# Kernel tuning notes

Measured on AMD Instinct MI355X. Metric: run time of the kernel, lower is better.

## Reference

```python
import jax, jax.numpy as jnp
import numpy as np

# ---- db4 filters (pywt conventions: dec_lo = rec_lo[::-1], rec_hi = qmf(rec_lo)) ----
F = 8  # db4 filter length
_rec_lo = np.array([0.23037781330885523, 0.7148465705525415, 0.6308807679295904,
                    -0.027983769416983849, -0.18703481171888114, 0.030841381835986965,
                    0.032883011666982945, -0.010597401784997278], dtype=np.float32)
_rec_hi = _rec_lo[::-1].copy()
_rec_hi[1::2] *= -1.0
REC_LO = jnp.asarray(_rec_lo)
REC_HI = jnp.asarray(_rec_hi)

MAX_LEVEL = 9  # pywt.dwt_max_level(4096, 8)


def _conv1d(x, kernel, stride=1, padding='VALID', lhs_dilation=None):
    # x: [B, L] -> correlation (XLA conv does NOT flip the kernel)
    out = jax.lax.conv_general_dilated(
        x[:, None, :], kernel[None, None, :],
        window_strides=(stride,), padding=padding,
        lhs_dilation=lhs_dilation,
        dimension_numbers=('NCH', 'OIH', 'NCH'))
    return out[:, 0, :]


def dwt(x):
    # pywt.dwt(x, 'db4', mode='symmetric'):
    # cA = np.convolve(sym_ext(x, F-1), dec_lo, 'valid')[1::2]
    # convolution with dec filter == correlation with rec filter (its reverse)
    ext = jnp.pad(x, ((0, 0), (F - 1, F - 1)), mode='symmetric')[:, 1:]
    return _conv1d(ext, REC_LO, stride=2), _conv1d(ext, REC_HI, stride=2)


def idwt(ca, cd):
    # pywt.idwt: zero-upsample coeffs, full convolution with rec filters, trim edges
    n = ca.shape[1]
    pad = ((F - 1, F - 1),)
    out = (_conv1d(ca, REC_LO[::-1], padding=pad, lhs_dilation=(2,)) +
           _conv1d(cd, REC_HI[::-1], padding=pad, lhs_dilation=(2,)))
    return out[:, F - 2:2 * n]  # output length = 2n - F + 2


def wavelet_features(x1):
    # Faithful to WaveletDWTLayer stack + WaveletParsingLayer: at each level k>=2,
    # reconstruct with details of levels k and k-1 only (others zeroed), with
    # pywt.waverec's trim-by-one rule; concatenate the 8 full-length reconstructions.
    a = x1
    cds, recs = [], []
    for level in range(1, MAX_LEVEL + 1):
        a, d = dwt(a)
        if level >= 2:
            r = idwt(jnp.zeros_like(d), d)
            for j in range(level - 2, -1, -1):
                dj = cds[j] if j == level - 2 else jnp.zeros_like(cds[j])
                if r.shape[1] == dj.shape[1] + 1:  # waverec trim rule
                    r = r[:, :-1]
                r = idwt(r, dj)
            recs.append(r)  # [B, signal_length]
        cds.append(d)
    return jnp.concatenate(recs, axis=1)  # [B, signal_length*(MAX_LEVEL-1)]


def reference(x1, x2, x3, W0, b0, W1, b1, W2, b2):
    # x2/x3 are placeholders in the original module (overwritten by layers 1/2)
    h = wavelet_features(x1)
    for W, b in ((W0, b0), (W1, b1), (W2, b2)):
        h = jax.nn.relu(h) @ W.T + b
    return h


def setup_inputs() -> dict:
    key = jax.random.key(0)
    ks = jax.random.split(key, 4)
    B, N = 2048, 4096
    D_IN, H1, H2, OUT = 32768, 181, 13, 10
    return {
        'x1': jax.random.normal(ks[0], (B, N), jnp.float32),
        'x2': jnp.zeros((B, 1, 8), jnp.float32),
        'x3': jnp.zeros((B, 1, 8), jnp.float32),
        'W0': jax.random.normal(ks[1], (H1, D_IN), jnp.float32) / np.float32(np.sqrt(D_IN)),
        'b0': jnp.zeros((H1,), jnp.float32),
        'W1': jax.random.normal(ks[2], (H2, H1), jnp.float32) / np.float32(np.sqrt(H1)),
        'b1': jnp.zeros((H2,), jnp.float32),
        'W2': jax.random.normal(ks[3], (OUT, H2), jnp.float32) / np.float32(np.sqrt(H2)),
        'b2': jnp.zeros((OUT,), jnp.float32),
    }
```

## Files before the change

### kernel.cpp

```cpp
#include <hip/hip_runtime.h>
#include <hip/hip_bf16.h>


typedef _Float16 f16x8 __attribute__((ext_vector_type(8)));
typedef _Float16 f16x4v __attribute__((ext_vector_type(4)));
typedef float f32x4 __attribute__((ext_vector_type(4)));

#define WV_THREADS 256
#define DROW 4144

#define L0 0.23037781330885523f
#define L1 0.7148465705525415f
#define L2f 0.6308807679295904f
#define L3 -0.02798376941698385f
#define L4 -0.18703481171888114f
#define L5 0.030841381835986965f
#define L6 0.032883011666982945f
#define L7 -0.010597401784997278f

#define H0 -0.010597401784997278f
#define H1 -0.032883011666982945f
#define H2 0.030841381835986965f
#define H3 0.18703481171888114f
#define H4 -0.02798376941698385f
#define H5 -0.6308807679295904f
#define H6 0.7148465705525415f
#define H7 -0.23037781330885523f

__device__ __forceinline__ int ext_idx(int j, int n) {
  return (j < 6) ? (5 - j) : ((j < n + 6) ? (j - 6) : (2 * n + 5 - j));
}

__device__ __forceinline__ void dwt2(const float* a, float* anext, float* d,
                                     int n, int m, bool store_a) {
  const int ng = (m + 1) >> 1;
  for (int g = threadIdx.x; g < ng; g += WV_THREADS) {
    float w[10];
    if (g >= 2 && 4 * g + 9 <= n + 5) {
      const float2* af = (const float2*)a + (2 * g - 3);
      float2 b0 = af[0], b1 = af[1], b2 = af[2], b3 = af[3], b4 = af[4];
      w[0] = b0.x; w[1] = b0.y; w[2] = b1.x; w[3] = b1.y; w[4] = b2.x;
      w[5] = b2.y; w[6] = b3.x; w[7] = b3.y; w[8] = b4.x; w[9] = b4.y;
    } else {
#pragma unroll
      for (int q = 0; q < 10; ++q) {
        int j = 4 * g + q;
        int jm = n + 12;
        if (j > jm) j = jm;
        w[q] = a[ext_idx(j, n)];
      }
    }
    float sl0 = w[0]*L0 + w[1]*L1 + w[2]*L2f + w[3]*L3 + w[4]*L4 + w[5]*L5 + w[6]*L6 + w[7]*L7;
    float sh0 = w[0]*H0 + w[1]*H1 + w[2]*H2  + w[3]*H3 + w[4]*H4 + w[5]*H5 + w[6]*H6 + w[7]*H7;
    float sl1 = w[2]*L0 + w[3]*L1 + w[4]*L2f + w[5]*L3 + w[6]*L4 + w[7]*L5 + w[8]*L6 + w[9]*L7;
    float sh1 = w[2]*H0 + w[3]*H1 + w[4]*H2  + w[5]*H3 + w[6]*H4 + w[7]*H5 + w[8]*H6 + w[9]*H7;
    if (2 * g + 1 < m) {
      if (store_a) *(float2*)(anext + 2 * g) = make_float2(sl0, sl1);
      *(float2*)(d + 2 * g) = make_float2(sh0, sh1);
    } else {
      if (store_a) anext[2 * g] = sl0;
      d[2 * g] = sh0;
    }
  }
}

template <bool HAS_CA, bool HAS_CD, bool FINAL>
__device__ __forceinline__ void idwt2(const float* ca, const float* cd,
                                      float* outl, _Float16* outg, int dlen) {
  const int npair = dlen - 3;
  const int ng = (npair + 1) >> 1;
  for (int g = threadIdx.x; g < ng; g += WV_THREADS) {
    float e0 = 0.f, o0 = 0.f, e1 = 0.f, o1 = 0.f;
    if (HAS_CA) {
      const float2* f = (const float2*)ca + g;
      float2 a0 = f[0], a1 = f[1], a2 = f[2];
      e0 = a1.y*L0 + a1.x*L2f + a0.y*L4 + a0.x*L6;
      o0 = a1.y*L1 + a1.x*L3  + a0.y*L5 + a0.x*L7;
      e1 = a2.x*L0 + a1.y*L2f + a1.x*L4 + a0.y*L6;
      o1 = a2.x*L1 + a1.y*L3  + a1.x*L5 + a0.y*L7;
    }
    if (HAS_CD) {
      const float2* f = (const float2*)cd + g;
      float2 d0 = f[0], d1 = f[1], d2 = f[2];
      e0 += d1.y*H0 + d1.x*H2 + d0.y*H4 + d0.x*H6;
      o0 += d1.y*H1 + d1.x*H3 + d0.y*H5 + d0.x*H7;
      e1 += d2.x*H0 + d1.y*H2 + d1.x*H4 + d0.y*H6;
      o1 += d2.x*H1 + d1.y*H3 + d1.x*H5 + d0.y*H7;
    }
    bool full = (2 * g + 1 < npair);
    if (FINAL) {
      if (full) {
        f16x4v h;
        h[0] = (_Float16)fmaxf(e0, 0.f); h[1] = (_Float16)fmaxf(o0, 0.f);
        h[2] = (_Float16)fmaxf(e1, 0.f); h[3] = (_Float16)fmaxf(o1, 0.f);
        *(f16x4v*)(outg + 4 * g) = h;
      } else {
        outg[4 * g]     = (_Float16)fmaxf(e0, 0.f);
        outg[4 * g + 1] = (_Float16)fmaxf(o0, 0.f);
      }
    } else {
      if (full) *(float4*)(outl + 4 * g) = make_float4(e0, o0, e1, o1);
      else      *(float2*)(outl + 4 * g) = make_float2(e0, o0);
    }
  }
}

__global__ __launch_bounds__(WV_THREADS) void wv_analysis_cvt(
    const float* __restrict__ x, float* __restrict__ dG,
    const float* __restrict__ W0, _Float16* __restrict__ Bw) {
  __shared__ float r1[4104];
  __shared__ float r2[2056];
  const int tid = threadIdx.x;

  if (blockIdx.x >= 2048) {
    size_t i = ((size_t)(blockIdx.x - 2048) * 256 + tid) * 4;
    int rowc = (int)(i >> 15);
    f16x4v h;
    if (rowc < 181) {
      const float4 v = *(const float4*)(W0 + i);
      h[0] = (_Float16)v.x; h[1] = (_Float16)v.y;
      h[2] = (_Float16)v.z; h[3] = (_Float16)v.w;
    } else {
      h[0] = (_Float16)0.f; h[1] = (_Float16)0.f;
      h[2] = (_Float16)0.f; h[3] = (_Float16)0.f;
    }
    *(f16x4v*)(Bw + i) = h;
    return;
  }

  const int NLa[10]  = {4096, 2051, 1029, 518, 262, 134, 70, 38, 22, 14};
  const int DOFF[10] = {0, 0, 2052, 3082, 3600, 3862, 3996, 4066, 4104, 4126};
  const int LOFF[10] = {0, 0, 1036, 520, 2068, 1040, 2332, 1176, 2404, 1216};
  const int row = blockIdx.x;

  const float4* xr = (const float4*)(x + (size_t)row * 4096);
  for (int i = tid; i < 1024; i += WV_THREADS) ((float4*)r1)[i] = xr[i];
  __syncthreads();

  float* dr = dG + (size_t)row * DROW;
  dwt2(r1, r2, dr + DOFF[1], NLa[0], NLa[1], true);
  __syncthreads();
  const float* ap = r2;
  float* an = r1;
  for (int lev = 2; lev <= 9; ++lev) {
    float* dbuf = ((lev & 1) ? r2 : r1) + LOFF[lev];
    dwt2(ap, an, dbuf, NLa[lev - 1], NLa[lev], lev < 9);
    __syncthreads();
    const float* t = ap; ap = an; an = (float*)t;
  }
  for (int lev = 2; lev <= 9; ++lev) {
    const float* src = ((lev & 1) ? r2 : r1) + LOFF[lev];
    float* dst = dr + DOFF[lev];
    for (int i = tid; i < NLa[lev]; i += WV_THREADS) dst[i] = src[i];
  }
}

__global__ __launch_bounds__(WV_THREADS, 6) void wv_synth(
    const float* __restrict__ dG, _Float16* __restrict__ A) {
  __shared__ float s1[2052];
  __shared__ float s2[2052];
  const int NLa[10]  = {4096, 2051, 1029, 518, 262, 134, 70, 38, 22, 14};
  const int DOFF[10] = {0, 0, 2052, 3082, 3600, 3862, 3996, 4066, 4104, 4126};
  const int row = blockIdx.x;
  const int L = 2 + blockIdx.y;
  const int tid = threadIdx.x;
  const float* dr = dG + (size_t)row * DROW;

  float* cur = s1;
  float* nxt = s2;
  int startj = L - 2;
  if (L >= 6) {
    if (tid < 64) {
      idwt2<false, true, false>(nullptr, dr + DOFF[L], cur, nullptr, NLa[L]);
      asm volatile("s_waitcnt lgkmcnt(0)" ::: "memory");
      for (int j = L - 2; j >= 5; --j) {
        if (j == L - 2)
          idwt2<true, true, false>(cur, dr + DOFF[j + 1], nxt, nullptr, NLa[j + 1]);
        else
          idwt2<true, false, false>(cur, nullptr, nxt, nullptr, NLa[j + 1]);
        asm volatile("s_waitcnt lgkmcnt(0)" ::: "memory");
        float* t = cur; cur = nxt; nxt = t;
      }
    } else {
      for (int j = L - 2; j >= 5; --j) { float* t = cur; cur = nxt; nxt = t; }
    }
    __syncthreads();
    startj = 4;
  } else {
    idwt2<false, true, false>(nullptr, dr + DOFF[L], cur, nullptr, NLa[L]);
    __syncthreads();
  }
  for (int j = startj; j >= 1; --j) {
    if (j == L - 2)
      idwt2<true, true, false>(cur, dr + DOFF[j + 1], nxt, nullptr, NLa[j + 1]);
    else
      idwt2<true, false, false>(cur, nullptr, nxt, nullptr, NLa[j + 1]);
    __syncthreads();
    float* t = cur; cur = nxt; nxt = t;
  }
  _Float16* og = A + (size_t)row * 32768 + (size_t)(L - 2) * 4096;
  if (L == 2)
    idwt2<true, true, true>(cur, dr + DOFF[1], nullptr, og, 2051);
  else
    idwt2<true, false, true>(cur, nullptr, nullptr, og, 2051);
}

__device__ __forceinline__ void load_lds16(const void* g, void* l) {
  __builtin_amdgcn_global_load_lds((__attribute__((address_space(1))) unsigned int*)g,
                                   (__attribute__((address_space(3))) unsigned int*)l,
                                   16, 0, 0);
}

__global__ __launch_bounds__(256, 2) void gemm_kernel(
    const _Float16* __restrict__ A, const _Float16* __restrict__ Bw,
    float* __restrict__ P, int kchunk) {
  __shared__ _Float16 As[128 * 64];
  __shared__ _Float16 Bs[192 * 64];
  const int tid = threadIdx.x;
  const int lane = tid & 63;
  const int wave = tid >> 6;
  const int m0 = blockIdx.x * 128;
  const int k0 = blockIdx.y * kchunk;
  const int nstages = kchunk >> 6;

  f32x4 acc[2][12];
#pragma unroll
  for (int mt = 0; mt < 2; ++mt)
#pragma unroll
    for (int nt = 0; nt < 12; ++nt) acc[mt][nt] = (f32x4){0.f, 0.f, 0.f, 0.f};

  for (int ks = 0; ks < nstages; ++ks) {
    const int kbase = k0 + (ks << 6);
    __syncthreads();
#pragma unroll
    for (int t = 0; t < 4; ++t) {
      int g = ((wave * 4 + t) << 6) + lane;
      int r = g >> 3, cs = g & 7;
      const _Float16* gp = A + (size_t)(m0 + r) * 32768 + kbase + ((cs ^ (r & 7)) << 3);
      load_lds16(gp, (char*)As + (size_t)((wave * 4 + t) << 10));
    }
#pragma unroll
    for (int t = 0; t < 6; ++t) {
      int g = ((wave * 6 + t) << 6) + lane;
      int r = g >> 3, cs = g & 7;
      const _Float16* gp = Bw + (size_t)r * 32768 + kbase + ((cs ^ (r & 7)) << 3);
      load_lds16(gp, (char*)Bs + (size_t)((wave * 6 + t) << 10));
    }
    __syncthreads();
#pragma unroll
    for (int kk = 0; kk < 2; ++kk) {
      const int chunk = kk * 4 + (lane >> 4);
      f16x8 af[2];
#pragma unroll
      for (int mt = 0; mt < 2; ++mt) {
        int r = wave * 32 + mt * 16 + (lane & 15);
        af[mt] = *(const f16x8*)(As + r * 64 + ((chunk ^ (r & 7)) << 3));
      }
#pragma unroll
      for (int nt = 0; nt < 12; ++nt) {
        int rb = nt * 16 + (lane & 15);
        f16x8 bf = *(const f16x8*)(Bs + rb * 64 + ((chunk ^ (rb & 7)) << 3));
        acc[0][nt] = __builtin_amdgcn_mfma_f32_16x16x32_f16(af[0], bf, acc[0][nt], 0, 0, 0);
        acc[1][nt] = __builtin_amdgcn_mfma_f32_16x16x32_f16(af[1], bf, acc[1][nt], 0, 0, 0);
      }
    }
  }
  float* Pp = P + ((size_t)blockIdx.y * 2048 + m0) * 192;
#pragma unroll
  for (int mt = 0; mt < 2; ++mt)
#pragma unroll
    for (int nt = 0; nt < 12; ++nt)
#pragma unroll
      for (int r4 = 0; r4 < 4; ++r4) {
        int rr = wave * 32 + mt * 16 + ((lane >> 4) << 2) + r4;
        int cc = nt * 16 + (lane & 15);
        Pp[(size_t)rr * 192 + cc] = acc[mt][nt][r4];
      }
}

__global__ __launch_bounds__(256) void mlp_kernel(
    const float* __restrict__ P, const float* __restrict__ b0,
    const float* __restrict__ W1, const float* __restrict__ b1,
    const float* __restrict__ W2, const float* __restrict__ b2,
    float* __restrict__ out, int nsplit) {
  __shared__ float part[4][193];
  __shared__ float h1[192];
  __shared__ float h2[13];
  const int row = blockIdx.x;
  const int t = threadIdx.x;
  const int g = t >> 6;
  const int l = t & 63;

  float a0 = 0.f, a1 = 0.f, a2 = 0.f;
  const int per = nsplit >> 2;
  for (int si = 0; si < per; ++si) {
    int s = g + (si << 2);
    const float* Pr = P + ((size_t)s * 2048 + row) * 192;
    a0 += Pr[l]; a1 += Pr[64 + l]; a2 += Pr[128 + l];
  }
  part[g][l] = a0; part[g][64 + l] = a1; part[g][128 + l] = a2;
  __syncthreads();

  if (t < 192) {
    float v = part[0][t] + part[1][t] + part[2][t] + part[3][t];
    h1[t] = (t < 181) ? fmaxf(v + b0[t], 0.f) : 0.f;
  }
  __syncthreads();

#pragma unroll
  for (int r = 0; r < 4; ++r) {
    int j = g + (r << 2);
    if (j < 13) {
      float v = 0.f;
#pragma unroll
      for (int q = 0; q < 3; ++q) {
        int n = l + (q << 6);
        if (n < 181) v += h1[n] * W1[j * 181 + n];
      }
      for (int off = 32; off >= 1; off >>= 1) v += __shfl_down(v, off);
      if (l == 0) h2[j] = fmaxf(v + b1[j], 0.f);
    }
  }
  __syncthreads();

  if (t < 10) {
    float c = b2[t];
#pragma unroll
    for (int j = 0; j < 13; ++j) c += h2[j] * W2[t * 13 + j];
    out[(size_t)row * 10 + t] = c;
  }
}

extern "C" void kernel_launch(void* const* d_in, const int* in_sizes, int n_in,
                              void* d_out, int out_size, void* d_ws, size_t ws_size,
                              hipStream_t stream) {
  const float* x1 = (const float*)d_in[0];
  const float* W0 = (const float*)d_in[3];
  const float* b0 = (const float*)d_in[4];
  const float* W1 = (const float*)d_in[5];
  const float* b1 = (const float*)d_in[6];
  const float* W2 = (const float*)d_in[7];
  const float* b2 = (const float*)d_in[8];
  float* out = (float*)d_out;

  char* ws = (char*)d_ws;
  const size_t A_BYTES = (size_t)2048 * 32768 * 2;
  const size_t B_BYTES = (size_t)192 * 32768 * 2;
  _Float16* Afeat = (_Float16*)ws;
  _Float16* Bw = (_Float16*)(ws + A_BYTES);
  float* Dq = (float*)(ws + A_BYTES + B_BYTES);
  float* P = (float*)(ws + A_BYTES + B_BYTES);

  int nsplit = 32;
  while (nsplit > 1 &&
         A_BYTES + B_BYTES + (size_t)nsplit * 2048 * 192 * 4 > ws_size)
    nsplit >>= 1;

  wv_analysis_cvt<<<2048 + 6144, WV_THREADS, 0, stream>>>(x1, Dq, W0, Bw);
  dim3 sg(2048, 8);
  wv_synth<<<sg, WV_THREADS, 0, stream>>>(Dq, Afeat);
  dim3 gg(16, nsplit);
  gemm_kernel<<<gg, 256, 0, stream>>>(Afeat, Bw, P, 32768 / nsplit);
  mlp_kernel<<<2048, 256, 0, stream>>>(P, b0, W1, b1, W2, b2, out, nsplit);
}
```

Baseline: 228.2 us.

## Fix GEMM split-K at 16 with swizzled block mapping, simplify synth, vectorize copies

Several changes land together. The GEMM split-K factor is now a compile-time constant of 16, replacing the runtime choice that picked up to 32 splits, and launches a 1D grid whose block index is remapped so consecutive blocks share an M tile across K chunks. The mlp kernel reads that constant too. The wavelet synthesis drops its single-wave path for deep levels and runs all levels with the full block, and the detail-coefficient copy in analysis now uses float2 stores. Fewer splits shrink the partial-sum traffic and the reduction work but give the GEMM fewer blocks (256) to spread across the GPU.

After: 243.1 us. 6.5% more time.

```diff
diff --git a/kernel.cpp b/kernel.cpp
--- a/kernel.cpp
+++ b/kernel.cpp
@@ -8,6 +8,8 @@
 
 #define WV_THREADS 256
 #define DROW 4144
+#define NSPLIT 16
+#define KCHUNK 2048
 
 #define L0 0.23037781330885523f
 #define L1 0.7148465705525415f
@@ -151,7 +153,10 @@
   for (int lev = 2; lev <= 9; ++lev) {
     const float* src = ((lev & 1) ? r2 : r1) + LOFF[lev];
     float* dst = dr + DOFF[lev];
-    for (int i = tid; i < NLa[lev]; i += WV_THREADS) dst[i] = src[i];
+    const int n = NLa[lev];
+    for (int i = 2 * tid; i + 1 < n; i += 2 * WV_THREADS)
+      *(float2*)(dst + i) = *(const float2*)(src + i);
+    if ((n & 1) && tid == 0) dst[n - 1] = src[n - 1];
   }
 }
 
@@ -163,34 +168,13 @@
   const int DOFF[10] = {0, 0, 2052, 3082, 3600, 3862, 3996, 4066, 4104, 4126};
   const int row = blockIdx.x;
   const int L = 2 + blockIdx.y;
-  const int tid = threadIdx.x;
   const float* dr = dG + (size_t)row * DROW;
 
+  idwt2<false, true, false>(nullptr, dr + DOFF[L], s1, nullptr, NLa[L]);
+  __syncthreads();
   float* cur = s1;
   float* nxt = s2;
-  int startj = L - 2;
-  if (L >= 6) {
-    if (tid < 64) {
-      idwt2<false, true, false>(nullptr, dr + DOFF[L], cur, nullptr, NLa[L]);
-      asm volatile("s_waitcnt lgkmcnt(0)" ::: "memory");
-      for (int j = L - 2; j >= 5; --j) {
-        if (j == L - 2)
-          idwt2<true, true, false>(cur, dr + DOFF[j + 1], nxt, nullptr, NLa[j + 1]);
-        else
-          idwt2<true, false, false>(cur, nullptr, nxt, nullptr, NLa[j + 1]);
-        asm volatile("s_waitcnt lgkmcnt(0)" ::: "memory");
-        float* t = cur; cur = nxt; nxt = t;
-      }
-    } else {
-      for (int j = L - 2; j >= 5; --j) { float* t = cur; cur = nxt; nxt = t; }
-    }
-    __syncthreads();
-    startj = 4;
-  } else {
-    idwt2<false, true, false>(nullptr, dr + DOFF[L], cur, nullptr, NLa[L]);
-    __syncthreads();
-  }
-  for (int j = startj; j >= 1; --j) {
+  for (int j = L - 2; j >= 1; --j) {
     if (j == L - 2)
       idwt2<true, true, false>(cur, dr + DOFF[j + 1], nxt, nullptr, NLa[j + 1]);
     else
@@ -213,15 +197,17 @@
 
 __global__ __launch_bounds__(256, 2) void gemm_kernel(
     const _Float16* __restrict__ A, const _Float16* __restrict__ Bw,
-    float* __restrict__ P, int kchunk) {
+    float* __restrict__ P) {
   __shared__ _Float16 As[128 * 64];
   __shared__ _Float16 Bs[192 * 64];
   const int tid = threadIdx.x;
   const int lane = tid & 63;
   const int wave = tid >> 6;
-  const int m0 = blockIdx.x * 128;
-  const int k0 = blockIdx.y * kchunk;
-  const int nstages = kchunk >> 6;
+  const int id = blockIdx.x;
+  const int k_idx = (id & 7) + 8 * ((id >> 3) >> 4);
+  const int m_idx = (id >> 3) & 15;
+  const int m0 = m_idx * 128;
+  const int k0 = k_idx * KCHUNK;
 
   f32x4 acc[2][12];
 #pragma unroll
@@ -229,7 +215,7 @@
 #pragma unroll
     for (int nt = 0; nt < 12; ++nt) acc[mt][nt] = (f32x4){0.f, 0.f, 0.f, 0.f};
 
-  for (int ks = 0; ks < nstages; ++ks) {
+  for (int ks = 0; ks < (KCHUNK >> 6); ++ks) {
     const int kbase = k0 + (ks << 6);
     __syncthreads();
 #pragma unroll
@@ -265,7 +251,7 @@
       }
     }
   }
-  float* Pp = P + ((size_t)blockIdx.y * 2048 + m0) * 192;
+  float* Pp = P + ((size_t)k_idx * 2048 + m0) * 192;
 #pragma unroll
   for (int mt = 0; mt < 2; ++mt)
 #pragma unroll
@@ -282,7 +268,7 @@
     const float* __restrict__ P, const float* __restrict__ b0,
     const float* __restrict__ W1, const float* __restrict__ b1,
     const float* __restrict__ W2, const float* __restrict__ b2,
-    float* __restrict__ out, int nsplit) {
+    float* __restrict__ out) {
   __shared__ float part[4][193];
   __shared__ float h1[192];
   __shared__ float h2[13];
@@ -292,8 +278,7 @@
   const int l = t & 63;
 
   float a0 = 0.f, a1 = 0.f, a2 = 0.f;
-  const int per = nsplit >> 2;
-  for (int si = 0; si < per; ++si) {
+  for (int si = 0; si < NSPLIT / 4; ++si) {
     int s = g + (si << 2);
     const float* Pr = P + ((size_t)s * 2048 + row) * 192;
     a0 += Pr[l]; a1 += Pr[64 + l]; a2 += Pr[128 + l];
@@ -351,15 +336,9 @@
   float* Dq = (float*)(ws + A_BYTES + B_BYTES);
   float* P = (float*)(ws + A_BYTES + B_BYTES);
 
-  int nsplit = 32;
-  while (nsplit > 1 &&
-         A_BYTES + B_BYTES + (size_t)nsplit * 2048 * 192 * 4 > ws_size)
-    nsplit >>= 1;
-
   wv_analysis_cvt<<<2048 + 6144, WV_THREADS, 0, stream>>>(x1, Dq, W0, Bw);
   dim3 sg(2048, 8);
   wv_synth<<<sg, WV_THREADS, 0, stream>>>(Dq, Afeat);
-  dim3 gg(16, nsplit);
-  gemm_kernel<<<gg, 256, 0, stream>>>(Afeat, Bw, P, 32768 / nsplit);
-  mlp_kernel<<<2048, 256, 0, stream>>>(P, b0, W1, b1, W2, b2, out, nsplit);
-}
+  gemm_kernel<<<16 * NSPLIT, 256, 0, stream>>>(Afeat, Bw, P);
+  mlp_kernel<<<2048, 256, 0, stream>>>(P, b0, W1, b1, W2, b2, out);
+}
```
